# Kernel optimization log

Hardware: AMD Instinct MI355X
Metric: run time of the kernel (lower is better)

## Reference

```python
import jax, jax.numpy as jnp
import numpy as np

B, C, N = 8, 128, 256          # batch, descriptor dim, num points
DIMS = [2 * C, 512, 256, 64, 1]  # [input_dim] + cfg.layers + [1]
EPS = 1e-5


def setup_inputs() -> dict:
    key = jax.random.key(0)
    ks = jax.random.split(key, 32)
    inp = {"x": jax.random.normal(ks[0], (B, C, N), dtype=jnp.float32)}
    ki = 1
    for li in range(4):
        cin, cout = DIMS[li], DIMS[li + 1]
        inp[f"W{li+1}"] = jax.random.normal(ks[ki], (cout, cin), dtype=jnp.float32) / np.sqrt(cin); ki += 1
        inp[f"b{li+1}"] = jnp.zeros((cout,), dtype=jnp.float32)
        if li < 3:  # BatchNorm only on hidden layers
            inp[f"g{li+1}"] = jnp.ones((cout,), dtype=jnp.float32)
            inp[f"be{li+1}"] = jnp.zeros((cout,), dtype=jnp.float32)
            inp[f"m{li+1}"] = 0.1 * jax.random.normal(ks[ki], (cout,), dtype=jnp.float32); ki += 1
            inp[f"v{li+1}"] = 0.5 + jax.random.uniform(ks[ki], (cout,), dtype=jnp.float32); ki += 1
    return inp


def _bn(h, g, be, m, v):
    # inference-mode BatchNorm1d over channel axis of (b, c, p)
    scale = (g * jax.lax.rsqrt(v + EPS))[None, :, None]
    return (h - m[None, :, None]) * scale + be[None, :, None]


def _conv1x1(h, W, b):
    # Conv1d kernel_size=1 == channel matmul: (o,c),(b,c,p)->(b,o,p)
    return jnp.einsum('oc,bcp->bop', W, h) + b[None, :, None]


def reference(x, W1, b1, g1, be1, m1, v1, W2, b2, g2, be2, m2, v2,
              W3, b3, g3, be3, m3, v3, W4, b4):
    b, c, n = x.shape
    # pairwise concat: inputs[:, :, i*n+j] = cat(x[:,:,i], x[:,:,j])
    xi = jnp.broadcast_to(x[:, :, :, None], (b, c, n, n))  # varies with i
    xj = jnp.broadcast_to(x[:, :, None, :], (b, c, n, n))  # varies with j
    pair = jnp.concatenate([xi, xj], axis=1).reshape(b, 2 * c, n * n)
    h = jax.nn.relu(_bn(_conv1x1(pair, W1, b1), g1, be1, m1, v1))
    h = jax.nn.relu(_bn(_conv1x1(h, W2, b2), g2, be2, m2, v2))
    h = jax.nn.relu(_bn(_conv1x1(h, W3, b3), g3, be3, m3, v3))
    h = _conv1x1(h, W4, b4)
    return jax.nn.sigmoid(h)  # (b, 1, n*n) == edges_pred
```

## Files before the change

### kernel.cpp

```cpp
#include <hip/hip_runtime.h>
#include <hip/hip_bf16.h>
#include <hip/hip_fp16.h>

typedef _Float16 f16x8 __attribute__((ext_vector_type(8)));
typedef _Float16 f16x4 __attribute__((ext_vector_type(4)));
typedef float    f32x4 __attribute__((ext_vector_type(4)));

#define EPSV 1e-5f

__global__ void prep_consts(
    const float* __restrict__ b1, const float* __restrict__ g1, const float* __restrict__ be1,
    const float* __restrict__ m1, const float* __restrict__ v1,
    const float* __restrict__ b2, const float* __restrict__ g2, const float* __restrict__ be2,
    const float* __restrict__ m2, const float* __restrict__ v2,
    const float* __restrict__ b3, const float* __restrict__ g3, const float* __restrict__ be3,
    const float* __restrict__ m3, const float* __restrict__ v3,
    float* __restrict__ sc1, float* __restrict__ sh1,
    float* __restrict__ sc2, float* __restrict__ sh2,
    float* __restrict__ sc3, float* __restrict__ sh3) {
  int t = threadIdx.x;
  if (t < 512) { float s = g1[t] * rsqrtf(v1[t] + EPSV); sc1[t] = s; sh1[t] = be1[t] + (b1[t] - m1[t]) * s; }
  if (t < 256) { float s = g2[t] * rsqrtf(v2[t] + EPSV); sc2[t] = s; sh2[t] = be2[t] + (b2[t] - m2[t]) * s; }
  if (t < 64)  { float s = g3[t] * rsqrtf(v3[t] + EPSV); sc3[t] = s; sh3[t] = be3[t] + (b3[t] - m3[t]) * s; }
}

__global__ void prep_convert(const float* __restrict__ W2, const float* __restrict__ W3,
                             _Float16* __restrict__ W2h, _Float16* __restrict__ W3h) {
  int idx = blockIdx.x * 256 + threadIdx.x;
  if (idx < 256 * 512) W2h[idx] = (_Float16)W2[idx];
  if (idx < 64 * 256)  W3h[idx] = (_Float16)W3[idx];
}

__global__ void prep_ab(const float* __restrict__ x, const float* __restrict__ W1,
                        const float* __restrict__ sc1, const float* __restrict__ sh1,
                        _Float16* __restrict__ Ap, _Float16* __restrict__ Bp) {
  int b  = blockIdx.x >> 7;
  int og = blockIdx.x & 127;
  int i  = threadIdx.x;
  float accA[4] = {0.f, 0.f, 0.f, 0.f};
  float accB[4] = {0.f, 0.f, 0.f, 0.f};
  const float* xb  = x  + (size_t)b * 128 * 256 + i;
  const float* w1r = W1 + (size_t)og * 4 * 256;
  for (int c = 0; c < 128; ++c) {
    float xa = xb[c * 256];
    #pragma unroll
    for (int oo = 0; oo < 4; ++oo) {
      accA[oo] = fmaf(w1r[oo * 256 + c],       xa, accA[oo]);
      accB[oo] = fmaf(w1r[oo * 256 + 128 + c], xa, accB[oo]);
    }
  }
  f16x4 oa, ob;
  {
    int o0 = og * 4;
    float4 s = *(const float4*)(sc1 + o0);
    float4 h = *(const float4*)(sh1 + o0);
    oa[0] = (_Float16)(accA[0] * s.x + h.x); oa[1] = (_Float16)(accA[1] * s.y + h.y);
    oa[2] = (_Float16)(accA[2] * s.z + h.z); oa[3] = (_Float16)(accA[3] * s.w + h.w);
    ob[0] = (_Float16)(accB[0] * s.x); ob[1] = (_Float16)(accB[1] * s.y);
    ob[2] = (_Float16)(accB[2] * s.z); ob[3] = (_Float16)(accB[3] * s.w);
  }
  size_t base = ((size_t)(b * 256 + i) << 9) + og * 4;
  *(f16x4*)(Ap + base) = oa;
  *(f16x4*)(Bp + base) = ob;
}

struct alignas(16) Smem {
  _Float16 sA[8][552];
  _Float16 sB[16][552];
  union {
    _Float16 W2s[2][256][40];
    struct { _Float16 h2[64][264]; float part[4][64]; } e;
  } u;
};

__global__ __launch_bounds__(512, 4) void edge_main(
    const _Float16* __restrict__ Ap, const _Float16* __restrict__ Bp,
    const _Float16* __restrict__ W2h, const _Float16* __restrict__ W3h,
    const float* __restrict__ sc2, const float* __restrict__ sh2,
    const float* __restrict__ sc3, const float* __restrict__ sh3,
    const float* __restrict__ W4, const float* __restrict__ b4,
    float* __restrict__ out) {
  __shared__ Smem sm;
  const int blk = blockIdx.x;
  const int b  = blk >> 9;
  const int it = (blk >> 4) & 31;
  const int jt = blk & 15;
  const int i0 = it * 8, j0 = jt * 16;

  const int t    = threadIdx.x;
  const int w    = t >> 6;
  const int lane = t & 63;
  const int llo  = lane & 15;
  const int lhi  = lane >> 4;
  const int chQ  = w & 3;
  const int ptH  = w >> 2;

  if (t < 256) {
    int r = t >> 5, c = (t & 31) * 16;
    const _Float16* src = Ap + ((size_t)(b * 256 + i0 + r) << 9) + c;
    *(f16x8*)&sm.sA[r][c]     = *(const f16x8*)(src);
    *(f16x8*)&sm.sA[r][c + 8] = *(const f16x8*)(src + 8);
  } else {
    int tt = t - 256;
    int r = tt >> 4, c = (tt & 15) * 32;
    const _Float16* src = Bp + ((size_t)(b * 256 + j0 + r) << 9) + c;
    #pragma unroll
    for (int s = 0; s < 4; ++s)
      *(f16x8*)&sm.sB[r][c + s * 8] = *(const f16x8*)(src + s * 8);
  }

  const int w2row = t >> 2;
  const int w2seg = (t & 3) * 8;
  const _Float16* w2gsrc = W2h + (size_t)w2row * 512 + w2seg;
  _Float16* w2dst0 = &sm.u.W2s[0][w2row][w2seg];
  _Float16* w2dst1 = &sm.u.W2s[0][w2row + 128][w2seg];

  {
    f16x8 p0 = *(const f16x8*)(w2gsrc);
    f16x8 p1 = *(const f16x8*)(w2gsrc + 65536);
    *(f16x8*)w2dst0 = p0;
    *(f16x8*)w2dst1 = p1;
  }

  const f32x4 vzero = {0.f, 0.f, 0.f, 0.f};
  f32x4 acc[4][4];
  #pragma unroll
  for (int mt = 0; mt < 4; ++mt)
    #pragma unroll
    for (int nt = 0; nt < 4; ++nt) acc[mt][nt] = vzero;

  const f16x8 z8 = {};

  __syncthreads();

  #pragma unroll 2
  for (int ks = 0; ks < 16; ++ks) {
    const int cur = ks & 1;
    const int k0 = ks * 32 + lhi * 8;

    f16x8 g0, g1;
    if (ks < 15) {
      g0 = *(const f16x8*)(w2gsrc + (ks + 1) * 32);
      g1 = *(const f16x8*)(w2gsrc + 65536 + (ks + 1) * 32);
    }

    f16x8 bv = *(const f16x8*)&sm.sB[llo][k0];
    f16x8 bfr[4];
    #pragma unroll
    for (int nt = 0; nt < 4; ++nt) {
      f16x8 av = *(const f16x8*)&sm.sA[ptH * 4 + nt][k0];
      f16x8 sv = av + bv;
      bfr[nt] = __builtin_elementwise_max(sv, z8);
    }

    __builtin_amdgcn_s_setprio(1);
    #pragma unroll
    for (int mt = 0; mt < 4; ++mt) {
      f16x8 af = *(const f16x8*)&sm.u.W2s[cur][chQ * 64 + mt * 16 + llo][lhi * 8];
      #pragma unroll
      for (int nt = 0; nt < 4; ++nt)
        acc[mt][nt] = __builtin_amdgcn_mfma_f32_16x16x32_f16(af, bfr[nt], acc[mt][nt], 0, 0, 0);
    }
    __builtin_amdgcn_s_setprio(0);

    if (ks < 15) {
      *(f16x8*)(w2dst0 + (cur ^ 1) * 10240) = g0;
      *(f16x8*)(w2dst1 + (cur ^ 1) * 10240) = g1;
    }
    __syncthreads();
  }

  #pragma unroll
  for (int pass = 0; pass < 2; ++pass) {
    if (ptH == pass) {
      #pragma unroll
      for (int mt = 0; mt < 4; ++mt) {
        int ch = chQ * 64 + mt * 16 + lhi * 4;
        float4 s = *(const float4*)(sc2 + ch);
        float4 h = *(const float4*)(sh2 + ch);
        #pragma unroll
        for (int nt = 0; nt < 4; ++nt) {
          int pt = nt * 16 + llo;
          f32x4 a = acc[mt][nt];
          f16x4 hb;
          hb[0] = (_Float16)fmaxf(fmaf(a[0], s.x, h.x), 0.f);
          hb[1] = (_Float16)fmaxf(fmaf(a[1], s.y, h.y), 0.f);
          hb[2] = (_Float16)fmaxf(fmaf(a[2], s.z, h.z), 0.f);
          hb[3] = (_Float16)fmaxf(fmaf(a[3], s.w, h.w), 0.f);
          *(f16x4*)&sm.u.e.h2[pt][ch] = hb;
        }
      }
    }
    __syncthreads();

    {
      const int chF = w & 3, ptS = w >> 2;
      f32x4 acc3[2];
      acc3[0] = vzero; acc3[1] = vzero;
      const _Float16* w3p = W3h + (size_t)(chF * 16 + llo) * 256 + lhi * 8;
      #pragma unroll
      for (int k8 = 0; k8 < 8; ++k8) {
        f16x8 a3 = *(const f16x8*)(w3p + k8 * 32);
        #pragma unroll
        for (int q2 = 0; q2 < 2; ++q2) {
          f16x8 b3 = *(const f16x8*)&sm.u.e.h2[(ptS * 2 + q2) * 16 + llo][k8 * 32 + lhi * 8];
          acc3[q2] = __builtin_amdgcn_mfma_f32_16x16x32_f16(a3, b3, acc3[q2], 0, 0, 0);
        }
      }
      int ch3 = chF * 16 + lhi * 4;
      float4 s  = *(const float4*)(sc3 + ch3);
      float4 h  = *(const float4*)(sh3 + ch3);
      float4 wv = *(const float4*)(W4 + ch3);
      #pragma unroll
      for (int q2 = 0; q2 < 2; ++q2) {
        float p = fmaxf(fmaf(acc3[q2][0], s.x, h.x), 0.f) * wv.x
                + fmaxf(fmaf(acc3[q2][1], s.y, h.y), 0.f) * wv.y
                + fmaxf(fmaf(acc3[q2][2], s.z, h.z), 0.f) * wv.z
                + fmaxf(fmaf(acc3[q2][3], s.w, h.w), 0.f) * wv.w;
        p += __shfl_xor(p, 16);
        p += __shfl_xor(p, 32);
        if (lane < 16) sm.u.e.part[chF][(ptS * 2 + q2) * 16 + llo] = p;
      }
    }
    __syncthreads();

    if (t < 64) {
      float tot = sm.u.e.part[0][t] + sm.u.e.part[1][t] + sm.u.e.part[2][t]
                + sm.u.e.part[3][t] + b4[0];
      float sg = 1.f / (1.f + __expf(-tot));
      int il = 4 * pass + (t >> 4), jl = t & 15;
      out[(size_t)b * 65536 + (size_t)(i0 + il) * 256 + (j0 + jl)] = sg;
    }
  }
}

extern "C" void kernel_launch(void* const* d_in, const int* in_sizes, int n_in,
                              void* d_out, int out_size, void* d_ws, size_t ws_size,
                              hipStream_t stream) {
  const float* x   = (const float*)d_in[0];
  const float* W1  = (const float*)d_in[1];
  const float* b1  = (const float*)d_in[2];
  const float* g1  = (const float*)d_in[3];
  const float* be1 = (const float*)d_in[4];
  const float* m1  = (const float*)d_in[5];
  const float* v1  = (const float*)d_in[6];
  const float* W2  = (const float*)d_in[7];
  const float* b2  = (const float*)d_in[8];
  const float* g2  = (const float*)d_in[9];
  const float* be2 = (const float*)d_in[10];
  const float* m2  = (const float*)d_in[11];
  const float* v2  = (const float*)d_in[12];
  const float* W3  = (const float*)d_in[13];
  const float* b3  = (const float*)d_in[14];
  const float* g3  = (const float*)d_in[15];
  const float* be3 = (const float*)d_in[16];
  const float* m3  = (const float*)d_in[17];
  const float* v3  = (const float*)d_in[18];
  const float* W4  = (const float*)d_in[19];
  const float* b4  = (const float*)d_in[20];

  _Float16* Ap = (_Float16*)d_ws;
  _Float16* Bp = Ap + 1048576;
  float* sc1 = (float*)(Bp + 1048576);
  float* sh1 = sc1 + 512;
  float* sc2 = sh1 + 512;
  float* sh2 = sc2 + 256;
  float* sc3 = sh2 + 256;
  float* sh3 = sc3 + 64;
  _Float16* W2h = (_Float16*)(sh3 + 64);
  _Float16* W3h = W2h + 131072;

  prep_consts<<<1, 512, 0, stream>>>(b1, g1, be1, m1, v1, b2, g2, be2, m2, v2,
                                     b3, g3, be3, m3, v3, sc1, sh1, sc2, sh2, sc3, sh3);
  prep_convert<<<512, 256, 0, stream>>>(W2, W3, W2h, W3h);
  prep_ab<<<1024, 256, 0, stream>>>(x, W1, sc1, sh1, Ap, Bp);
  edge_main<<<4096, 512, 0, stream>>>(Ap, Bp, W2h, W3h, sc2, sh2, sc3, sh3, W4, b4, (float*)d_out);
}
```

Before: 199.6 us.

## Pre-swizzle W2 into MFMA fragment order and load it directly from global

```diff
diff --git a/kernel.cpp b/kernel.cpp
--- a/kernel.cpp
+++ b/kernel.cpp
@@ -25,10 +25,19 @@
 }
 
 __global__ void prep_convert(const float* __restrict__ W2, const float* __restrict__ W3,
-                             _Float16* __restrict__ W2h, _Float16* __restrict__ W3h) {
-  int idx = blockIdx.x * 256 + threadIdx.x;
-  if (idx < 256 * 512) W2h[idx] = (_Float16)W2[idx];
-  if (idx < 64 * 256)  W3h[idx] = (_Float16)W3[idx];
+                             _Float16* __restrict__ W2T, _Float16* __restrict__ W3h) {
+  int tid = blockIdx.x * 256 + threadIdx.x;
+  {
+    int lane = tid & 63, cg = (tid >> 6) & 15, ks = tid >> 10;
+    int ch = cg * 16 + (lane & 15);
+    int k  = ks * 32 + (lane >> 4) * 8;
+    const float* src = W2 + (size_t)ch * 512 + k;
+    f16x8 v;
+    #pragma unroll
+    for (int e = 0; e < 8; ++e) v[e] = (_Float16)src[e];
+    *(f16x8*)(W2T + (size_t)tid * 8) = v;
+  }
+  W3h[tid] = (_Float16)W3[tid];
 }
 
 __global__ void prep_ab(const float* __restrict__ x, const float* __restrict__ W1,
@@ -65,17 +74,15 @@
 }
 
 struct alignas(16) Smem {
-  _Float16 sA[8][552];
-  _Float16 sB[16][552];
   union {
-    _Float16 W2s[2][256][40];
+    struct { _Float16 sA[8][552]; _Float16 sB[16][552]; } s2;
     struct { _Float16 h2[64][264]; float part[4][64]; } e;
   } u;
 };
 
 __global__ __launch_bounds__(512, 4) void edge_main(
     const _Float16* __restrict__ Ap, const _Float16* __restrict__ Bp,
-    const _Float16* __restrict__ W2h, const _Float16* __restrict__ W3h,
+    const _Float16* __restrict__ W2T, const _Float16* __restrict__ W3h,
     const float* __restrict__ sc2, const float* __restrict__ sh2,
     const float* __restrict__ sc3, const float* __restrict__ sh3,
     const float* __restrict__ W4, const float* __restrict__ b4,
@@ -98,28 +105,15 @@
   if (t < 256) {
     int r = t >> 5, c = (t & 31) * 16;
     const _Float16* src = Ap + ((size_t)(b * 256 + i0 + r) << 9) + c;
-    *(f16x8*)&sm.sA[r][c]     = *(const f16x8*)(src);
-    *(f16x8*)&sm.sA[r][c + 8] = *(const f16x8*)(src + 8);
+    *(f16x8*)&sm.u.s2.sA[r][c]     = *(const f16x8*)(src);
+    *(f16x8*)&sm.u.s2.sA[r][c + 8] = *(const f16x8*)(src + 8);
   } else {
     int tt = t - 256;
     int r = tt >> 4, c = (tt & 15) * 32;
     const _Float16* src = Bp + ((size_t)(b * 256 + j0 + r) << 9) + c;
     #pragma unroll
     for (int s = 0; s < 4; ++s)
-      *(f16x8*)&sm.sB[r][c + s * 8] = *(const f16x8*)(src + s * 8);
-  }
-
-  const int w2row = t >> 2;
-  const int w2seg = (t & 3) * 8;
-  const _Float16* w2gsrc = W2h + (size_t)w2row * 512 + w2seg;
-  _Float16* w2dst0 = &sm.u.W2s[0][w2row][w2seg];
-  _Float16* w2dst1 = &sm.u.W2s[0][w2row + 128][w2seg];
-
-  {
-    f16x8 p0 = *(const f16x8*)(w2gsrc);
-    f16x8 p1 = *(const f16x8*)(w2gsrc + 65536);
-    *(f16x8*)w2dst0 = p0;
-    *(f16x8*)w2dst1 = p1;
+      *(f16x8*)&sm.u.s2.sB[r][c + s * 8] = *(const f16x8*)(src + s * 8);
   }
 
   const f32x4 vzero = {0.f, 0.f, 0.f, 0.f};
@@ -130,45 +124,38 @@
     for (int nt = 0; nt < 4; ++nt) acc[mt][nt] = vzero;
 
   const f16x8 z8 = {};
+  const _Float16* w2p = W2T + chQ * 2048 + lane * 8;
 
   __syncthreads();
 
   #pragma unroll 2
   for (int ks = 0; ks < 16; ++ks) {
-    const int cur = ks & 1;
+    f16x8 af[4];
+    #pragma unroll
+    for (int mt = 0; mt < 4; ++mt)
+      af[mt] = *(const f16x8*)(w2p + mt * 512);
+    w2p += 8192;
+
     const int k0 = ks * 32 + lhi * 8;
-
-    f16x8 g0, g1;
-    if (ks < 15) {
-      g0 = *(const f16x8*)(w2gsrc + (ks + 1) * 32);
-      g1 = *(const f16x8*)(w2gsrc + 65536 + (ks + 1) * 32);
-    }
-
-    f16x8 bv = *(const f16x8*)&sm.sB[llo][k0];
+    f16x8 bv = *(const f16x8*)&sm.u.s2.sB[llo][k0];
     f16x8 bfr[4];
     #pragma unroll
     for (int nt = 0; nt < 4; ++nt) {
-      f16x8 av = *(const f16x8*)&sm.sA[ptH * 4 + nt][k0];
+      f16x8 av = *(const f16x8*)&sm.u.s2.sA[ptH * 4 + nt][k0];
       f16x8 sv = av + bv;
       bfr[nt] = __builtin_elementwise_max(sv, z8);
     }
 
     __builtin_amdgcn_s_setprio(1);
     #pragma unroll
-    for (int mt = 0; mt < 4; ++mt) {
-      f16x8 af = *(const f16x8*)&sm.u.W2s[cur][chQ * 64 + mt * 16 + llo][lhi * 8];
+    for (int mt = 0; mt < 4; ++mt)
       #pragma unroll
       for (int nt = 0; nt < 4; ++nt)
-        acc[mt][nt] = __builtin_amdgcn_mfma_f32_16x16x32_f16(af, bfr[nt], acc[mt][nt], 0, 0, 0);
-    }
+        acc[mt][nt] = __builtin_amdgcn_mfma_f32_16x16x32_f16(af[mt], bfr[nt], acc[mt][nt], 0, 0, 0);
     __builtin_amdgcn_s_setprio(0);
-
-    if (ks < 15) {
-      *(f16x8*)(w2dst0 + (cur ^ 1) * 10240) = g0;
-      *(f16x8*)(w2dst1 + (cur ^ 1) * 10240) = g1;
-    }
-    __syncthreads();
-  }
+  }
+
+  __syncthreads();
 
   #pragma unroll
   for (int pass = 0; pass < 2; ++pass) {
@@ -231,6 +218,7 @@
       int il = 4 * pass + (t >> 4), jl = t & 15;
       out[(size_t)b * 65536 + (size_t)(i0 + il) * 256 + (j0 + jl)] = sg;
     }
+    __syncthreads();
   }
 }
 
@@ -267,12 +255,12 @@
   float* sh2 = sc2 + 256;
   float* sc3 = sh2 + 256;
   float* sh3 = sc3 + 64;
-  _Float16* W2h = (_Float16*)(sh3 + 64);
-  _Float16* W3h = W2h + 131072;
+  _Float16* W2T = (_Float16*)(sh3 + 64);
+  _Float16* W3h = W2T + 131072;
 
   prep_consts<<<1, 512, 0, stream>>>(b1, g1, be1, m1, v1, b2, g2, be2, m2, v2,
                                      b3, g3, be3, m3, v3, sc1, sh1, sc2, sh2, sc3, sh3);
-  prep_convert<<<512, 256, 0, stream>>>(W2, W3, W2h, W3h);
+  prep_convert<<<64, 256, 0, stream>>>(W2, W3, W2T, W3h);
   prep_ab<<<1024, 256, 0, stream>>>(x, W1, sc1, sh1, Ap, Bp);
-  edge_main<<<4096, 512, 0, stream>>>(Ap, Bp, W2h, W3h, sc2, sh2, sc3, sh3, W4, b4, (float*)d_out);
-}
+  edge_main<<<4096, 512, 0, stream>>>(Ap, Bp, W2T, W3h, sc2, sh2, sc3, sh3, W4, b4, (float*)d_out);
+}
```

Result: faster. 189.7 us (-4.9%).
